# Optimization experiments

Measured on AMD Instinct MI355X. Metric: run time of the kernel, lower is better.

The kernel has to match this reference:

```python
import jax, jax.numpy as jnp
import numpy as np

B = 131072
H_GAS = 8
H_EXT = 16
# gas order and net counts, total 99 tiny MLPs
GAS_SIZES = [23, 29, 13, 9, 3, 9, 13]  # h2o, h2o_sq, o3, co2, n2o, ch4, u
N_NETS = 29

# index maps taken verbatim from the 29 tau_gases assignment lines
H2O_ROWS = np.arange(23)
H2O_IDX = np.array([0,1,2,3,4,5,6,3,4,9,10,11,12,13,14,15,16,17,18,19,20,21,22])
O3_ROWS = np.array([0,1,2,17,18,19,20,21,22,25,26,27,28])
CO2_ROWS = np.array([0,1,2,5,6,9,10,13,14])
N2O_ROWS = np.array([0,1,2])
CH4_ROWS = np.array([0,1,2,3,4,7,8,11,12])
U_ROWS = np.array([0,1,2,15,16,17,18,19,20,21,22,27,28])


def setup_inputs() -> dict:
    key = jax.random.key(0)
    ks = jax.random.split(key, 23)
    f = jnp.float32
    inp = {
        'temp': jax.random.normal(ks[0], (B, 1), f),
        'pressure': jax.random.normal(ks[1], (B, 1), f),
        'comp_h2o': jax.random.uniform(ks[2], (B, 1), f),
        'comp_h2o_sq': jax.random.uniform(ks[3], (B, 1), f),
        'comp_o3': jax.random.uniform(ks[4], (B, 1), f),
        'comp_co2': jax.random.uniform(ks[5], (B, 1), f),
        'comp_n2o': jax.random.uniform(ks[6], (B, 1), f),
        'comp_ch4': jax.random.uniform(ks[7], (B, 1), f),
        'comp_u': jax.random.uniform(ks[8], (B, 1), f),
        'lwp': jax.random.uniform(ks[9], (B, 1), f, minval=0.05, maxval=1.0),
        'iwp': jax.random.uniform(ks[10], (B, 1), f, minval=0.05, maxval=1.0),
        'mu': jax.random.uniform(ks[11], (B, 1), f, minval=0.1, maxval=1.0),
        'mu_bar': jax.random.uniform(ks[12], (B, 1), f, minval=0.1, maxval=1.0),
        'gas_W1': jax.random.normal(ks[13], (99, 2, H_GAS), f) * 0.5,
        'gas_b1': jax.random.normal(ks[14], (99, H_GAS), f) * 0.1,
        'gas_W2': jax.random.normal(ks[15], (99, H_GAS, 1), f) * 0.5,
        'gas_b2': jax.random.uniform(ks[16], (99, 1), f, minval=0.05, maxval=0.5),
        'lw_w': jax.random.uniform(ks[17], (N_NETS, 1), f, minval=0.05, maxval=1.0),
        'iw_w': jax.random.uniform(ks[18], (N_NETS, 1), f, minval=0.05, maxval=1.0),
        'ext_W1': jax.random.normal(ks[19], (N_NETS, 4, H_EXT), f) * 0.5,
        'ext_b1': jax.random.normal(ks[20], (N_NETS, H_EXT), f) * 0.1,
        'ext_W2': jax.random.normal(ks[21], (N_NETS, H_EXT, 3), f) * 0.5,
        'ext_b2': jax.random.normal(ks[22], (N_NETS, 3), f) * 0.1,
    }
    return inp


def reference(temp, pressure, comp_h2o, comp_h2o_sq, comp_o3, comp_co2, comp_n2o,
              comp_ch4, comp_u, lwp, iwp, mu, mu_bar,
              gas_W1, gas_b1, gas_W2, gas_b2, lw_w, iw_w,
              ext_W1, ext_b1, ext_W2, ext_b2):
    b = temp.shape[0]
    X = jnp.concatenate([temp, pressure], axis=-1)              # [B,2]
    # all 99 per-gas tiny MLPs in one batched pass
    h = jax.nn.elu(jnp.einsum('bi,nih->nbh', X, gas_W1) + gas_b1[:, None, :])
    ke = jax.nn.relu(jnp.einsum('nbh,nho->nbo', h, gas_W2) + gas_b2[:, None, :])[..., 0]  # [99,B]
    comps = [comp_h2o, comp_h2o_sq, comp_o3, comp_co2, comp_n2o, comp_ch4, comp_u]
    comp_all = jnp.concatenate(
        [jnp.broadcast_to(c[:, 0][None, :], (n, b)) for c, n in zip(comps, GAS_SIZES)], axis=0)
    tau_all = ke * comp_all                                      # [99,B]
    h2o    = tau_all[0:23]
    h2o_sq = tau_all[23:52]
    o3     = tau_all[52:65]
    co2    = tau_all[65:74]
    n2o    = tau_all[74:77]
    ch4    = tau_all[77:86]
    u      = tau_all[86:99]
    # scatter-combine into the 29 spectral channels
    tau_g = h2o_sq                                               # every row has h2o_sq[k]
    tau_g = tau_g.at[H2O_ROWS].add(h2o[H2O_IDX])
    tau_g = tau_g.at[O3_ROWS].add(o3)
    tau_g = tau_g.at[CO2_ROWS].add(co2)
    tau_g = tau_g.at[N2O_ROWS].add(n2o)
    tau_g = tau_g.at[CH4_ROWS].add(ch4)
    tau_g = tau_g.at[U_ROWS].add(u)
    tau_lw = lw_w * lwp[:, 0][None, :]                           # [29,B]
    tau_iw = iw_w * iwp[:, 0][None, :]
    tau_total = tau_g + tau_lw + tau_iw
    in1 = tau_lw / tau_total
    in2 = tau_iw / tau_total
    mu_v, mub_v = mu[:, 0], mu_bar[:, 0]
    in3_dir = tau_total / mu_v[None, :]
    in3_dif = tau_total / mub_v[None, :]

    def ext(i1, i2, i3, m):
        Xe = jnp.stack([i1, i2, i3, jnp.broadcast_to(m[None, :], i1.shape)], axis=-1)  # [29,B,4]
        he = jax.nn.elu(jnp.einsum('nbi,nih->nbh', Xe, ext_W1) + ext_b1[:, None, :])
        return jax.nn.relu(jnp.einsum('nbh,nho->nbo', he, ext_W2) + ext_b2[:, None, :])

    e_direct = jax.nn.softmax(ext(in1, in2, in3_dir, mu_v), axis=-1)   # [29,B,3]
    e_diffuse = jax.nn.softmax(ext(in1, in2, in3_dif, mub_v), axis=-1)
    t_direct = jnp.exp(-in3_dir)
    t_diffuse = jnp.exp(-in3_dif)
    return (t_direct, t_diffuse, e_direct, e_diffuse)
```

## Files before the change

kernel.cpp:

```cpp
#include <hip/hip_runtime.h>
#include <math.h>

#define TPB 256

constexpr int ROW_START[30] = {
    0, 7, 14, 21, 24, 27, 30, 33, 36, 39, 42, 45, 48, 51, 54, 57, 60,
    63, 67, 71, 75, 79, 83, 87, 88, 89, 91, 93, 96, 99};

constexpr int NET_ID[99] = {
    23, 0, 52, 65, 74, 77, 86,
    24, 1, 53, 66, 75, 78, 87,
    25, 2, 54, 67, 76, 79, 88,
    26, 3, 80,
    27, 4, 81,
    28, 5, 68,
    29, 6, 69,
    30, 3, 82,
    31, 4, 83,
    32, 9, 70,
    33, 10, 71,
    34, 11, 84,
    35, 12, 85,
    36, 13, 72,
    37, 14, 73,
    38, 15, 89,
    39, 16, 90,
    40, 17, 55, 91,
    41, 18, 56, 92,
    42, 19, 57, 93,
    43, 20, 58, 94,
    44, 21, 59, 95,
    45, 22, 60, 96,
    46,
    47,
    48, 61,
    49, 62,
    50, 63, 97,
    51, 64, 98};

constexpr int COMP_ID[99] = {
    1, 0, 2, 3, 4, 5, 6,
    1, 0, 2, 3, 4, 5, 6,
    1, 0, 2, 3, 4, 5, 6,
    1, 0, 5,
    1, 0, 5,
    1, 0, 3,
    1, 0, 3,
    1, 0, 5,
    1, 0, 5,
    1, 0, 3,
    1, 0, 3,
    1, 0, 5,
    1, 0, 5,
    1, 0, 3,
    1, 0, 3,
    1, 0, 6,
    1, 0, 6,
    1, 0, 2, 6,
    1, 0, 2, 6,
    1, 0, 2, 6,
    1, 0, 2, 6,
    1, 0, 2, 6,
    1, 0, 2, 6,
    1,
    1,
    1, 2,
    1, 2,
    1, 2, 6,
    1, 2, 6};

__device__ __forceinline__ float fast_rcp(float x) {
    return __builtin_amdgcn_rcpf(x);
}

__device__ __forceinline__ float elu(float h) {
    return fmaxf(h, __expf(fminf(h, 0.f)) - 1.f);
}

template <int R>
__device__ __forceinline__ float gas_row(
    float t, float p, const float* comp,
    const float* __restrict__ gW1, const float* __restrict__ gb1,
    const float* __restrict__ gW2, const float* __restrict__ gb2)
{
    float tg = 0.f;
    #pragma unroll
    for (int i = ROW_START[R]; i < ROW_START[R + 1]; ++i) {
        const int n = NET_ID[i];
        const float c = comp[COMP_ID[i]];
        const float* w1 = gW1 + n * 16;
        const float* b1 = gb1 + n * 8;
        const float* w2 = gW2 + n * 8;
        float acc = gb2[n];
        #pragma unroll
        for (int j = 0; j < 8; ++j) {
            float h = fmaf(t, w1[j], fmaf(p, w1[8 + j], b1[j]));
            acc = fmaf(elu(h), w2[j], acc);
        }
        tg = fmaf(fmaxf(acc, 0.f), c, tg);
    }
    return tg;
}

__global__ __launch_bounds__(TPB) void atm_kernel(
    const float* __restrict__ temp,
    const float* __restrict__ pressure,
    const float* __restrict__ c_h2o,
    const float* __restrict__ c_h2o_sq,
    const float* __restrict__ c_o3,
    const float* __restrict__ c_co2,
    const float* __restrict__ c_n2o,
    const float* __restrict__ c_ch4,
    const float* __restrict__ c_u,
    const float* __restrict__ lwp,
    const float* __restrict__ iwp,
    const float* __restrict__ mu,
    const float* __restrict__ mu_bar,
    const float* __restrict__ gW1,
    const float* __restrict__ gb1,
    const float* __restrict__ gW2,
    const float* __restrict__ gb2,
    const float* __restrict__ lw_w,
    const float* __restrict__ iw_w,
    const float* __restrict__ eW1,
    const float* __restrict__ eb1,
    const float* __restrict__ eW2,
    const float* __restrict__ eb2,
    float* __restrict__ out,
    int Bn)
{
    const int r = blockIdx.y;
    const long long b = (long long)blockIdx.x * TPB + threadIdx.x;
    if (b >= Bn) return;

    const float t = temp[b];
    const float p = pressure[b];
    float comp[7];
    comp[0] = c_h2o[b];
    comp[1] = c_h2o_sq[b];
    comp[2] = c_o3[b];
    comp[3] = c_co2[b];
    comp[4] = c_n2o[b];
    comp[5] = c_ch4[b];
    comp[6] = c_u[b];
    const float lwp_b = lwp[b], iwp_b = iwp[b];
    const float mu_b = mu[b], mub_b = mu_bar[b];

    float tau_g = 0.f;
    switch (r) {
#define ROW_CASE(R) case R: tau_g = gas_row<R>(t, p, comp, gW1, gb1, gW2, gb2); break;
        ROW_CASE(0)  ROW_CASE(1)  ROW_CASE(2)  ROW_CASE(3)  ROW_CASE(4)
        ROW_CASE(5)  ROW_CASE(6)  ROW_CASE(7)  ROW_CASE(8)  ROW_CASE(9)
        ROW_CASE(10) ROW_CASE(11) ROW_CASE(12) ROW_CASE(13) ROW_CASE(14)
        ROW_CASE(15) ROW_CASE(16) ROW_CASE(17) ROW_CASE(18) ROW_CASE(19)
        ROW_CASE(20) ROW_CASE(21) ROW_CASE(22) ROW_CASE(23) ROW_CASE(24)
        ROW_CASE(25) ROW_CASE(26) ROW_CASE(27) ROW_CASE(28)
#undef ROW_CASE
        default: break;
    }

    const float tlw = lw_w[r] * lwp_b;
    const float tiw = iw_w[r] * iwp_b;
    const float tau_tot = tau_g + tlw + tiw;
    const float inv_tt = fast_rcp(tau_tot);
    const float in1 = tlw * inv_tt;
    const float in2 = tiw * inv_tt;
    const float in3_dir = tau_tot * fast_rcp(mu_b);
    const float in3_dif = tau_tot * fast_rcp(mub_b);

    const size_t idx = (size_t)r * (size_t)Bn + (size_t)b;
    out[idx] = __expf(-in3_dir);
    out[(size_t)29 * Bn + idx] = __expf(-in3_dif);

    const float* w1  = eW1 + r * 64;
    const float* bb1 = eb1 + r * 16;
    const float* w2  = eW2 + r * 48;
    const float b20 = eb2[r * 3 + 0], b21 = eb2[r * 3 + 1], b22 = eb2[r * 3 + 2];

    float od0 = b20, od1 = b21, od2 = b22;
    float of0 = b20, of1 = b21, of2 = b22;
    #pragma unroll
    for (int j = 0; j < 16; ++j) {
        const float wj0 = w1[j];
        const float wj1 = w1[16 + j];
        const float wj2 = w1[32 + j];
        const float wj3 = w1[48 + j];
        const float bj  = bb1[j];
        const float u0 = w2[3 * j + 0];
        const float u1 = w2[3 * j + 1];
        const float u2 = w2[3 * j + 2];
        const float base = fmaf(in1, wj0, fmaf(in2, wj1, bj));
        {
            const float h = elu(fmaf(mu_b, wj3, fmaf(in3_dir, wj2, base)));
            od0 = fmaf(h, u0, od0);
            od1 = fmaf(h, u1, od1);
            od2 = fmaf(h, u2, od2);
        }
        {
            const float h = elu(fmaf(mub_b, wj3, fmaf(in3_dif, wj2, base)));
            of0 = fmaf(h, u0, of0);
            of1 = fmaf(h, u1, of1);
            of2 = fmaf(h, u2, of2);
        }
    }

    float* pd = out + (size_t)58 * Bn + idx * 3;
    {
        const float a0 = fmaxf(od0, 0.f), a1 = fmaxf(od1, 0.f), a2 = fmaxf(od2, 0.f);
        const float mx = fmaxf(a0, fmaxf(a1, a2));
        const float e0 = __expf(a0 - mx), e1 = __expf(a1 - mx), e2 = __expf(a2 - mx);
        const float rs = fast_rcp(e0 + e1 + e2);
        pd[0] = e0 * rs; pd[1] = e1 * rs; pd[2] = e2 * rs;
    }
    float* pf = out + (size_t)145 * Bn + idx * 3;
    {
        const float a0 = fmaxf(of0, 0.f), a1 = fmaxf(of1, 0.f), a2 = fmaxf(of2, 0.f);
        const float mx = fmaxf(a0, fmaxf(a1, a2));
        const float e0 = __expf(a0 - mx), e1 = __expf(a1 - mx), e2 = __expf(a2 - mx);
        const float rs = fast_rcp(e0 + e1 + e2);
        pf[0] = e0 * rs; pf[1] = e1 * rs; pf[2] = e2 * rs;
    }
}

extern "C" void kernel_launch(void* const* d_in, const int* in_sizes, int n_in,
                              void* d_out, int out_size, void* d_ws, size_t ws_size,
                              hipStream_t stream) {
    const int Bn = in_sizes[0];
    dim3 grid((Bn + TPB - 1) / TPB, 29);
    atm_kernel<<<grid, TPB, 0, stream>>>(
        (const float*)d_in[0],  (const float*)d_in[1],  (const float*)d_in[2],
        (const float*)d_in[3],  (const float*)d_in[4],  (const float*)d_in[5],
        (const float*)d_in[6],  (const float*)d_in[7],  (const float*)d_in[8],
        (const float*)d_in[9],  (const float*)d_in[10], (const float*)d_in[11],
        (const float*)d_in[12], (const float*)d_in[13], (const float*)d_in[14],
        (const float*)d_in[15], (const float*)d_in[16], (const float*)d_in[17],
        (const float*)d_in[18], (const float*)d_in[19], (const float*)d_in[20],
        (const float*)d_in[21], (const float*)d_in[22],
        (float*)d_out, Bn);
}
```

Before: 230.4 us.

## Process two batch elements per thread with vectorized loads/stores and row-major grid

Each thread now handles two consecutive batch elements, so the per-row weights it loads are reused across both and inputs and outputs move as float2. The grid is reordered so blockIdx.x indexes the 29 rows and blockIdx.y the batch chunk, which places blocks for all rows of the same batch slice next to each other and may improve input cache reuse. This raises register pressure and halves the thread count, and the float2 accesses assume an even batch size with 8-byte alignment.

```diff
diff --git a/kernel.cpp b/kernel.cpp
--- a/kernel.cpp
+++ b/kernel.cpp
@@ -2,6 +2,7 @@
 #include <math.h>
 
 #define TPB 256
+#define EPT 2
 
 constexpr int ROW_START[30] = {
     0, 7, 14, 21, 24, 27, 30, 33, 36, 39, 42, 45, 48, 51, 54, 57, 60,
@@ -78,28 +79,43 @@
 }
 
 template <int R>
-__device__ __forceinline__ float gas_row(
-    float t, float p, const float* comp,
+__device__ __forceinline__ void gas_row(
+    const float t[EPT], const float p[EPT], const float comp[7][EPT],
     const float* __restrict__ gW1, const float* __restrict__ gb1,
-    const float* __restrict__ gW2, const float* __restrict__ gb2)
+    const float* __restrict__ gW2, const float* __restrict__ gb2,
+    float tg[EPT])
 {
-    float tg = 0.f;
+    #pragma unroll
+    for (int e = 0; e < EPT; ++e) tg[e] = 0.f;
     #pragma unroll
     for (int i = ROW_START[R]; i < ROW_START[R + 1]; ++i) {
         const int n = NET_ID[i];
-        const float c = comp[COMP_ID[i]];
+        const int c = COMP_ID[i];
         const float* w1 = gW1 + n * 16;
         const float* b1 = gb1 + n * 8;
         const float* w2 = gW2 + n * 8;
-        float acc = gb2[n];
+        float acc[EPT];
+        #pragma unroll
+        for (int e = 0; e < EPT; ++e) acc[e] = gb2[n];
         #pragma unroll
         for (int j = 0; j < 8; ++j) {
-            float h = fmaf(t, w1[j], fmaf(p, w1[8 + j], b1[j]));
-            acc = fmaf(elu(h), w2[j], acc);
-        }
-        tg = fmaf(fmaxf(acc, 0.f), c, tg);
-    }
-    return tg;
+            const float a0 = w1[j], a1 = w1[8 + j], bj = b1[j], w2j = w2[j];
+            #pragma unroll
+            for (int e = 0; e < EPT; ++e) {
+                float h = fmaf(t[e], a0, fmaf(p[e], a1, bj));
+                acc[e] = fmaf(elu(h), w2j, acc[e]);
+            }
+        }
+        #pragma unroll
+        for (int e = 0; e < EPT; ++e)
+            tg[e] = fmaf(fmaxf(acc[e], 0.f), comp[c][e], tg[e]);
+    }
+}
+
+__device__ __forceinline__ void load2(const float* __restrict__ p, long long b0,
+                                      float v[EPT]) {
+    const float2 q = *(const float2*)(p + b0);
+    v[0] = q.x; v[1] = q.y;
 }
 
 __global__ __launch_bounds__(TPB) void atm_kernel(
@@ -129,26 +145,29 @@
     float* __restrict__ out,
     int Bn)
 {
-    const int r = blockIdx.y;
-    const long long b = (long long)blockIdx.x * TPB + threadIdx.x;
-    if (b >= Bn) return;
-
-    const float t = temp[b];
-    const float p = pressure[b];
-    float comp[7];
-    comp[0] = c_h2o[b];
-    comp[1] = c_h2o_sq[b];
-    comp[2] = c_o3[b];
-    comp[3] = c_co2[b];
-    comp[4] = c_n2o[b];
-    comp[5] = c_ch4[b];
-    comp[6] = c_u[b];
-    const float lwp_b = lwp[b], iwp_b = iwp[b];
-    const float mu_b = mu[b], mub_b = mu_bar[b];
-
-    float tau_g = 0.f;
+    const int r = blockIdx.x;
+    const long long vb = (long long)blockIdx.y * TPB + threadIdx.x;
+    const long long b0 = vb * EPT;
+    if (b0 >= Bn) return;
+
+    float t[EPT], p[EPT], comp[7][EPT], lwpv[EPT], iwpv[EPT], muv[EPT], mubv[EPT];
+    load2(temp,     b0, t);
+    load2(pressure, b0, p);
+    load2(c_h2o,    b0, comp[0]);
+    load2(c_h2o_sq, b0, comp[1]);
+    load2(c_o3,     b0, comp[2]);
+    load2(c_co2,    b0, comp[3]);
+    load2(c_n2o,    b0, comp[4]);
+    load2(c_ch4,    b0, comp[5]);
+    load2(c_u,      b0, comp[6]);
+    load2(lwp,      b0, lwpv);
+    load2(iwp,      b0, iwpv);
+    load2(mu,       b0, muv);
+    load2(mu_bar,   b0, mubv);
+
+    float tau_g[EPT];
     switch (r) {
-#define ROW_CASE(R) case R: tau_g = gas_row<R>(t, p, comp, gW1, gb1, gW2, gb2); break;
+#define ROW_CASE(R) case R: gas_row<R>(t, p, comp, gW1, gb1, gW2, gb2, tau_g); break;
         ROW_CASE(0)  ROW_CASE(1)  ROW_CASE(2)  ROW_CASE(3)  ROW_CASE(4)
         ROW_CASE(5)  ROW_CASE(6)  ROW_CASE(7)  ROW_CASE(8)  ROW_CASE(9)
         ROW_CASE(10) ROW_CASE(11) ROW_CASE(12) ROW_CASE(13) ROW_CASE(14)
@@ -159,26 +178,34 @@
         default: break;
     }
 
-    const float tlw = lw_w[r] * lwp_b;
-    const float tiw = iw_w[r] * iwp_b;
-    const float tau_tot = tau_g + tlw + tiw;
-    const float inv_tt = fast_rcp(tau_tot);
-    const float in1 = tlw * inv_tt;
-    const float in2 = tiw * inv_tt;
-    const float in3_dir = tau_tot * fast_rcp(mu_b);
-    const float in3_dif = tau_tot * fast_rcp(mub_b);
-
-    const size_t idx = (size_t)r * (size_t)Bn + (size_t)b;
-    out[idx] = __expf(-in3_dir);
-    out[(size_t)29 * Bn + idx] = __expf(-in3_dif);
+    const float lwr = lw_w[r], iwr = iw_w[r];
+    float in1[EPT], in2[EPT], i3d[EPT], i3f[EPT], td[EPT], tf[EPT];
+    #pragma unroll
+    for (int e = 0; e < EPT; ++e) {
+        const float tlw = lwr * lwpv[e];
+        const float tiw = iwr * iwpv[e];
+        const float tt  = tau_g[e] + tlw + tiw;
+        const float inv = fast_rcp(tt);
+        in1[e] = tlw * inv;
+        in2[e] = tiw * inv;
+        i3d[e] = tt * fast_rcp(muv[e]);
+        i3f[e] = tt * fast_rcp(mubv[e]);
+        td[e]  = __expf(-i3d[e]);
+        tf[e]  = __expf(-i3f[e]);
+    }
 
     const float* w1  = eW1 + r * 64;
     const float* bb1 = eb1 + r * 16;
     const float* w2  = eW2 + r * 48;
     const float b20 = eb2[r * 3 + 0], b21 = eb2[r * 3 + 1], b22 = eb2[r * 3 + 2];
 
-    float od0 = b20, od1 = b21, od2 = b22;
-    float of0 = b20, of1 = b21, of2 = b22;
+    float od[EPT][3], of[EPT][3];
+    #pragma unroll
+    for (int e = 0; e < EPT; ++e) {
+        od[e][0] = b20; od[e][1] = b21; od[e][2] = b22;
+        of[e][0] = b20; of[e][1] = b21; of[e][2] = b22;
+    }
+
     #pragma unroll
     for (int j = 0; j < 16; ++j) {
         const float wj0 = w1[j];
@@ -189,44 +216,57 @@
         const float u0 = w2[3 * j + 0];
         const float u1 = w2[3 * j + 1];
         const float u2 = w2[3 * j + 2];
-        const float base = fmaf(in1, wj0, fmaf(in2, wj1, bj));
+        #pragma unroll
+        for (int e = 0; e < EPT; ++e) {
+            const float base = fmaf(in1[e], wj0, fmaf(in2[e], wj1, bj));
+            const float hd = elu(fmaf(muv[e],  wj3, fmaf(i3d[e], wj2, base)));
+            od[e][0] = fmaf(hd, u0, od[e][0]);
+            od[e][1] = fmaf(hd, u1, od[e][1]);
+            od[e][2] = fmaf(hd, u2, od[e][2]);
+            const float hf = elu(fmaf(mubv[e], wj3, fmaf(i3f[e], wj2, base)));
+            of[e][0] = fmaf(hf, u0, of[e][0]);
+            of[e][1] = fmaf(hf, u1, of[e][1]);
+            of[e][2] = fmaf(hf, u2, of[e][2]);
+        }
+    }
+
+    float smd[EPT][3], smf[EPT][3];
+    #pragma unroll
+    for (int e = 0; e < EPT; ++e) {
         {
-            const float h = elu(fmaf(mu_b, wj3, fmaf(in3_dir, wj2, base)));
-            od0 = fmaf(h, u0, od0);
-            od1 = fmaf(h, u1, od1);
-            od2 = fmaf(h, u2, od2);
+            const float a0 = fmaxf(od[e][0], 0.f), a1 = fmaxf(od[e][1], 0.f), a2 = fmaxf(od[e][2], 0.f);
+            const float mx = fmaxf(a0, fmaxf(a1, a2));
+            const float e0 = __expf(a0 - mx), e1 = __expf(a1 - mx), e2 = __expf(a2 - mx);
+            const float rs = fast_rcp(e0 + e1 + e2);
+            smd[e][0] = e0 * rs; smd[e][1] = e1 * rs; smd[e][2] = e2 * rs;
         }
         {
-            const float h = elu(fmaf(mub_b, wj3, fmaf(in3_dif, wj2, base)));
-            of0 = fmaf(h, u0, of0);
-            of1 = fmaf(h, u1, of1);
-            of2 = fmaf(h, u2, of2);
-        }
-    }
-
+            const float a0 = fmaxf(of[e][0], 0.f), a1 = fmaxf(of[e][1], 0.f), a2 = fmaxf(of[e][2], 0.f);
+            const float mx = fmaxf(a0, fmaxf(a1, a2));
+            const float e0 = __expf(a0 - mx), e1 = __expf(a1 - mx), e2 = __expf(a2 - mx);
+            const float rs = fast_rcp(e0 + e1 + e2);
+            smf[e][0] = e0 * rs; smf[e][1] = e1 * rs; smf[e][2] = e2 * rs;
+        }
+    }
+
+    const size_t idx = (size_t)r * (size_t)Bn + (size_t)b0;
+    *(float2*)(out + idx)                    = make_float2(td[0], td[1]);
+    *(float2*)(out + (size_t)29 * Bn + idx)  = make_float2(tf[0], tf[1]);
     float* pd = out + (size_t)58 * Bn + idx * 3;
-    {
-        const float a0 = fmaxf(od0, 0.f), a1 = fmaxf(od1, 0.f), a2 = fmaxf(od2, 0.f);
-        const float mx = fmaxf(a0, fmaxf(a1, a2));
-        const float e0 = __expf(a0 - mx), e1 = __expf(a1 - mx), e2 = __expf(a2 - mx);
-        const float rs = fast_rcp(e0 + e1 + e2);
-        pd[0] = e0 * rs; pd[1] = e1 * rs; pd[2] = e2 * rs;
-    }
+    ((float2*)pd)[0] = make_float2(smd[0][0], smd[0][1]);
+    ((float2*)pd)[1] = make_float2(smd[0][2], smd[1][0]);
+    ((float2*)pd)[2] = make_float2(smd[1][1], smd[1][2]);
     float* pf = out + (size_t)145 * Bn + idx * 3;
-    {
-        const float a0 = fmaxf(of0, 0.f), a1 = fmaxf(of1, 0.f), a2 = fmaxf(of2, 0.f);
-        const float mx = fmaxf(a0, fmaxf(a1, a2));
-        const float e0 = __expf(a0 - mx), e1 = __expf(a1 - mx), e2 = __expf(a2 - mx);
-        const float rs = fast_rcp(e0 + e1 + e2);
-        pf[0] = e0 * rs; pf[1] = e1 * rs; pf[2] = e2 * rs;
-    }
+    ((float2*)pf)[0] = make_float2(smf[0][0], smf[0][1]);
+    ((float2*)pf)[1] = make_float2(smf[0][2], smf[1][0]);
+    ((float2*)pf)[2] = make_float2(smf[1][1], smf[1][2]);
 }
 
 extern "C" void kernel_launch(void* const* d_in, const int* in_sizes, int n_in,
                               void* d_out, int out_size, void* d_ws, size_t ws_size,
                               hipStream_t stream) {
     const int Bn = in_sizes[0];
-    dim3 grid((Bn + TPB - 1) / TPB, 29);
+    dim3 grid(29, (Bn + TPB * EPT - 1) / (TPB * EPT));
     atm_kernel<<<grid, TPB, 0, stream>>>(
         (const float*)d_in[0],  (const float*)d_in[1],  (const float*)d_in[2],
         (const float*)d_in[3],  (const float*)d_in[4],  (const float*)d_in[5],
```

New measurement: 227.7 us. Within noise of the previous version (-1.2%).
